# Kernel optimization log

Hardware: AMD Instinct MI355X
Metric: run time of the kernel (lower is better)

## Reference

```python
import jax, jax.numpy as jnp
import numpy as np
from jax import lax

B, D, H, FF, M = 256, 256, 8, 1024, 2048
HD = D // H
SCALE = 1.0 / np.sqrt(HD).astype(np.float32)
THR, MOM, LR = 0.5, 0.9, 0.1


def setup_inputs() -> dict:
    key = jax.random.key(0)
    ks = jax.random.split(key, 8)
    w = lambda k, sh: jax.random.normal(k, sh, dtype=jnp.float32) * 0.02
    return {
        "src": jax.random.normal(ks[0], (B, D), dtype=jnp.float32),
        "memory": jax.random.normal(ks[1], (M, D), dtype=jnp.float32) * 0.1,
        "momentum": jnp.zeros((M, D), jnp.float32),
        "scores": jax.random.uniform(ks[2], (M,), dtype=jnp.float32),
        "in_proj_w": w(ks[3], (3 * D, D)), "in_proj_b": jnp.zeros((3 * D,), jnp.float32),
        "out_w": w(ks[4], (D, D)), "out_b": jnp.zeros((D,), jnp.float32),
        "w1": w(ks[5], (FF, D)), "b1": jnp.zeros((FF,), jnp.float32),
        "w2": w(ks[6], (D, FF)), "b2": jnp.zeros((D,), jnp.float32),
        "g1": jnp.ones((D,), jnp.float32), "be1": jnp.zeros((D,), jnp.float32),
        "g2": jnp.ones((D,), jnp.float32), "be2": jnp.zeros((D,), jnp.float32),
        "ptr": M,
    }


def _ln(x, g, b):
    m = x.mean(-1, keepdims=True)
    v = ((x - m) ** 2).mean(-1, keepdims=True)
    return (x - m) / jnp.sqrt(v + 1e-5) * g + b


def reference(src, memory, momentum, scores, in_proj_w, in_proj_b, out_w, out_b,
              w1, b1, w2, b2, g1, be1, g2, be2, ptr):
    # --- surprise: 1 - max cosine similarity to memory slots ---
    xn = src / jnp.maximum(jnp.linalg.norm(src, axis=-1, keepdims=True), 1e-8)
    mn = memory / jnp.maximum(jnp.linalg.norm(memory, axis=-1, keepdims=True), 1e-8)
    sims = xn @ mn.T                                    # [B, M]
    surprises = jnp.where(jnp.linalg.norm(memory) == 0.0,
                          jnp.ones((B,), src.dtype), 1.0 - sims.max(-1))
    # --- self-attention; only the last (src) query row is used ---
    Wq, Wk, Wv = jnp.split(in_proj_w, 3, axis=0)
    bq, bk, bv = jnp.split(in_proj_b, 3, axis=0)
    q = (src @ Wq.T + bq).reshape(B, H, HD)             # [B,H,HD]
    k_mem = (memory @ Wk.T + bk).reshape(M, H, HD)      # shared across batch
    v_mem = (memory @ Wv.T + bv).reshape(M, H, HD)
    k_src = (src @ Wk.T + bk).reshape(B, H, HD)
    v_src = (src @ Wv.T + bv).reshape(B, H, HD)
    logits_mem = jnp.einsum('bhd,mhd->bhm', q, k_mem) * SCALE   # [B,H,M]
    logit_self = (q * k_src).sum(-1) * SCALE                    # [B,H]
    logits = jnp.concatenate([logits_mem, logit_self[..., None]], -1)  # [B,H,M+1]
    attn = jax.nn.softmax(logits, axis=-1)
    ctx = jnp.einsum('bhm,mhd->bhd', attn[..., :M], v_mem) + attn[..., M, None] * v_src
    attn_out = ctx.reshape(B, D) @ out_w.T + out_b
    h = _ln(src + attn_out, g1, be1)
    # --- sequential memory scatter update (detached in original) ---
    x_det = lax.stop_gradient(h)
    s_det = lax.stop_gradient(surprises)

    def step(carry, inp):
        mem, mom, sc, p = carry
        xi, si = inp
        cond = (si > THR) | (p < M)
        idx = jnp.mod(p, M)
        diff = xi - mem[idx]
        new_mom = MOM * mom[idx] + (1.0 - MOM) * diff
        mem = mem.at[idx].add(jnp.where(cond, LR * new_mom, 0.0))
        mom = mom.at[idx].set(jnp.where(cond, new_mom, mom[idx]))
        sc = sc.at[idx].set(jnp.where(cond, si, sc[idx]))
        return (mem, mom, sc, p + cond.astype(jnp.int32)), None

    (mem_f, mom_f, sc_f, _), _ = lax.scan(
        step, (memory, momentum, scores, jnp.int32(ptr)), (x_det, s_det))
    # --- FFN ---
    ff = jax.nn.relu(h @ w1.T + b1) @ w2.T + b2
    out = _ln(h + ff, g2, be2)
    return out, mem_f, mom_f, sc_f
```

## Files before the change

kernel.cpp:

```cpp
#include <hip/hip_runtime.h>
#include <math.h>

#define SCALE_F 0.17677669529663687f

typedef __attribute__((ext_vector_type(8))) short short8;
typedef __attribute__((ext_vector_type(4))) short short4v;
typedef __attribute__((ext_vector_type(4))) float f32x4;

__device__ inline short tobf(float x) {
    unsigned u = __float_as_uint(x);
    unsigned r = (u + 0x7FFFu + ((u >> 16) & 1u)) >> 16;
    return (short)r;
}
__device__ inline float frombf(short s) {
    return __uint_as_float(((unsigned)(unsigned short)s) << 16);
}

__device__ __forceinline__ short8 cv8(const float* __restrict__ p, int lo) {
    float4 a = *(const float4*)p, b = *(const float4*)(p + 4);
    float xs[8] = {a.x, a.y, a.z, a.w, b.x, b.y, b.z, b.w};
    short8 o;
    #pragma unroll
    for (int i = 0; i < 8; i++) {
        short hi = tobf(xs[i]);
        o[i] = lo ? tobf(xs[i] - frombf(hi)) : hi;
    }
    return o;
}

__device__ __forceinline__ void gemm_cv(short* lds,
    const float* __restrict__ A, int lda, int aLo,
    const float* __restrict__ B, int ldb, int bLo,
    float* Cf, short* Cb, int ldc, const float* bias, int transC, int bx, int by)
{
    short* Al = lds;
    short* Bl = lds + 2560;
    int t = threadIdx.x, w = t >> 6, l = t & 63;
    int r0 = by * 64, c0 = bx * 64;
    int srow = t >> 2, scol = (t & 3) * 8;
    f32x4 acc[4] = {{0.f,0.f,0.f,0.f},{0.f,0.f,0.f,0.f},{0.f,0.f,0.f,0.f},{0.f,0.f,0.f,0.f}};
    for (int kk = 0; kk < 256; kk += 32) {
        *(short8*)&Al[srow * 40 + scol] = cv8(A + (long long)(r0 + srow) * lda + kk + scol, aLo);
        *(short8*)&Bl[srow * 40 + scol] = cv8(B + (long long)(c0 + srow) * ldb + kk + scol, bLo);
        __syncthreads();
        short8 af = *(const short8*)&Al[(w * 16 + (l & 15)) * 40 + (l >> 4) * 8];
        #pragma unroll
        for (int j = 0; j < 4; j++) {
            short8 bf = *(const short8*)&Bl[(j * 16 + (l & 15)) * 40 + (l >> 4) * 8];
            acc[j] = __builtin_amdgcn_mfma_f32_16x16x32_bf16(af, bf, acc[j], 0, 0, 0);
        }
        __syncthreads();
    }
    int lc = l & 15, lr = (l >> 4) * 4;
    #pragma unroll
    for (int j = 0; j < 4; j++) {
        int col = c0 + j * 16 + lc;
        float bv = bias ? bias[col] : 0.f;
        #pragma unroll
        for (int r = 0; r < 4; r++) {
            int row = r0 + w * 16 + lr + r;
            float v = acc[j][r] + bv;
            long long idx = transC ? (long long)col * ldc + row : (long long)row * ldc + col;
            if (Cf) Cf[idx] = v;
            else    Cb[idx] = tobf(v);
        }
    }
}

__global__ __launch_bounds__(256) void proj_k(
    const float* __restrict__ src, const float* __restrict__ memory,
    const float* __restrict__ ipw, const float* __restrict__ ipb,
    const float* __restrict__ out_w, const float* __restrict__ w1, const float* __restrict__ w2,
    float* __restrict__ simdot_p, short* __restrict__ qkv_bf,
    short* __restrict__ k_bf, short* __restrict__ vt_bf,
    short* __restrict__ outw_bf, short* __restrict__ w1_bf, short* __restrict__ w2_bf,
    float* __restrict__ nx, float* __restrict__ nm, float* __restrict__ nm2)
{
    __shared__ short lds[5120];
    int bid = blockIdx.x, t = threadIdx.x, w = t >> 6, l = t & 63;
    if (bid < 384) {
        int tm = bid >> 7, r = bid & 127;
        int aLo = (tm == 2), bLo = (tm == 1);
        gemm_cv(lds, src, 256, aLo, memory, 256, bLo,
                simdot_p + (long long)tm * 524288, nullptr, 2048, nullptr, 0, r & 31, r >> 5);
    } else if (bid < 512) {
        int r = bid - 384;
        gemm_cv(lds, memory, 256, 0, ipw + 65536, 256, 0,
                nullptr, k_bf, 256, ipb + 256, 0, r & 3, r >> 2);
    } else if (bid < 640) {
        int r = bid - 512;
        gemm_cv(lds, memory, 256, 0, ipw + 131072, 256, 0,
                nullptr, vt_bf, 2048, ipb + 512, 1, r & 3, r >> 2);
    } else if (bid < 688) {
        int r = bid - 640;
        gemm_cv(lds, src, 256, 0, ipw, 256, 0,
                nullptr, qkv_bf, 768, ipb, 0, r % 12, r / 12);
    } else if (bid < 724) {
        int nb = bid - 688;
        #pragma unroll
        for (int i = 0; i < 16; i++) {
            int r = nb * 64 + i * 4 + w;
            bool issrc = r < 256;
            int rr = issrc ? r : r - 256;
            const float* rowp = issrc ? src + (long long)rr * 256 : memory + (long long)rr * 256;
            float4 x = *(const float4*)(rowp + l * 4);
            float ss = x.x * x.x + x.y * x.y + x.z * x.z + x.w * x.w;
            #pragma unroll
            for (int m = 32; m; m >>= 1) ss += __shfl_xor(ss, m, 64);
            if (l == 0) {
                if (issrc) nx[rr] = fmaxf(sqrtf(ss), 1e-8f);
                else { nm[rr] = fmaxf(sqrtf(ss), 1e-8f); nm2[rr] = ss; }
            }
        }
    } else {
        long long base = (long long)(bid - 724) * 4096 + t * 8;
        #pragma unroll
        for (int rep = 0; rep < 2; rep++) {
            long long e = base + rep * 2048;
            const float* sp; short* dp; long long off;
            if (e < 65536)       { sp = out_w; dp = outw_bf; off = e; }
            else if (e < 327680) { sp = w1;    dp = w1_bf;   off = e - 65536; }
            else                 { sp = w2;    dp = w2_bf;   off = e - 327680; }
            *(short8*)&dp[off] = cv8(sp + off, 0);
        }
    }
}

__global__ __launch_bounds__(256) void flash_sur_k(
    const short* __restrict__ qkv_bf, const short* __restrict__ k_bf,
    const short* __restrict__ vt_bf,
    float* __restrict__ pvpart, float* __restrict__ mpart, float* __restrict__ lpart,
    const float* __restrict__ simdot_p, const float* __restrict__ nx,
    const float* __restrict__ nm, const float* __restrict__ nm2, float* __restrict__ sur)
{
    __shared__ __align__(16) short smem[22016];
    int bid = blockIdx.x, t = threadIdx.x;
    if (bid >= 256) {
        float* red = (float*)smem;
        int b = bid - 256;
        float tot = 0.f;
        for (int m = t; m < 2048; m += 256) tot += nm2[m];
        red[t] = tot; __syncthreads();
        for (int s = 128; s; s >>= 1) { if (t < s) red[t] += red[t + s]; __syncthreads(); }
        float total = red[0];
        __syncthreads();
        float invx = 1.f / nx[b];
        float mx = -1e30f;
        for (int m = t; m < 2048; m += 256) {
            long long i = (long long)b * 2048 + m;
            float d = simdot_p[i] + simdot_p[524288 + i] + simdot_p[1048576 + i];
            mx = fmaxf(mx, d * invx / nm[m]);
        }
        red[t] = mx; __syncthreads();
        for (int s = 128; s; s >>= 1) { if (t < s) red[t] = fmaxf(red[t], red[t + s]); __syncthreads(); }
        if (t == 0) sur[b] = (total == 0.f) ? 1.f : 1.f - red[0];
        return;
    }
    int ms = bid & 7, h = (bid >> 3) & 7, qt = bid >> 6;
    int q0 = qt * 64, m0 = ms * 256;
    int S = bid & 63;
    int w = t >> 6, l = t & 63;
    short* Kl = smem;
    short* Pl = smem + 5120;
    short8 af = *(const short8*)(qkv_bf + (q0 + w * 16 + (l & 15)) * 768 + h * 32 + (l >> 4) * 8);
    f32x4 accL[16];
    #pragma unroll
    for (int j = 0; j < 16; j++) accL[j] = f32x4{0.f, 0.f, 0.f, 0.f};
    #pragma unroll
    for (int half = 0; half < 2; half++) {
        #pragma unroll
        for (int s = 0; s < 2; s++) {
            int seg = t + s * 256; int row = seg >> 2, off = (seg & 3) * 8;
            *(short8*)&Kl[row * 40 + off] =
                *(const short8*)(k_bf + (long long)(m0 + half * 128 + row) * 256 + h * 32 + off);
        }
        __syncthreads();
        #pragma unroll
        for (int j = 0; j < 8; j++) {
            short8 bf = *(const short8*)&Kl[(j * 16 + (l & 15)) * 40 + (l >> 4) * 8];
            accL[half * 8 + j] = __builtin_amdgcn_mfma_f32_16x16x32_bf16(af, bf, accL[half * 8 + j], 0, 0, 0);
        }
        __syncthreads();
    }
    int r4 = (l >> 4) * 4;
    float mloc[4], lsum[4];
    #pragma unroll
    for (int r = 0; r < 4; r++) {
        float mx = -1e30f;
        #pragma unroll
        for (int j = 0; j < 16; j++) mx = fmaxf(mx, accL[j][r] * SCALE_F);
        #pragma unroll
        for (int msk = 1; msk < 16; msk <<= 1) mx = fmaxf(mx, __shfl_xor(mx, msk, 64));
        mloc[r] = mx;
    }
    #pragma unroll
    for (int j = 0; j < 16; j++)
        #pragma unroll
        for (int r = 0; r < 4; r++)
            accL[j][r] = __expf(accL[j][r] * SCALE_F - mloc[r]);
    #pragma unroll
    for (int r = 0; r < 4; r++) {
        float ls = 0.f;
        #pragma unroll
        for (int j = 0; j < 16; j++) ls += accL[j][r];
        #pragma unroll
        for (int msk = 1; msk < 16; msk <<= 1) ls += __shfl_xor(ls, msk, 64);
        lsum[r] = ls;
    }
    if ((l & 15) == 0) {
        #pragma unroll
        for (int r = 0; r < 4; r++) {
            int gq = q0 + w * 16 + r4 + r;
            mpart[S * 256 + gq] = mloc[r];
            lpart[S * 256 + gq] = lsum[r];
        }
    }
    #pragma unroll
    for (int j = 0; j < 16; j++)
        #pragma unroll
        for (int r = 0; r < 4; r++)
            Pl[(w * 16 + r4 + r) * 264 + j * 16 + (l & 15)] = tobf(accL[j][r]);
    __syncthreads();
    f32x4 accP[2] = {{0.f,0.f,0.f,0.f},{0.f,0.f,0.f,0.f}};
    #pragma unroll
    for (int ks = 0; ks < 8; ks++) {
        short8 pa = *(const short8*)&Pl[(w * 16 + (l & 15)) * 264 + ks * 32 + (l >> 4) * 8];
        #pragma unroll
        for (int df = 0; df < 2; df++) {
            short8 vb = *(const short8*)(vt_bf + (long long)(h * 32 + df * 16 + (l & 15)) * 2048
                                         + m0 + ks * 32 + (l >> 4) * 8);
            accP[df] = __builtin_amdgcn_mfma_f32_16x16x32_bf16(pa, vb, accP[df], 0, 0, 0);
        }
    }
    #pragma unroll
    for (int df = 0; df < 2; df++)
        #pragma unroll
        for (int r = 0; r < 4; r++) {
            int gq = q0 + w * 16 + r4 + r;
            pvpart[((long long)S * 256 + gq) * 32 + df * 16 + (l & 15)] = accP[df][r];
        }
}

__global__ __launch_bounds__(256) void attn_gemm_k(
    const short* __restrict__ qkv_bf, const float* __restrict__ mpart,
    const float* __restrict__ lpart, const float* __restrict__ pvpart,
    const short* __restrict__ outw_bf, float* __restrict__ attn_part,
    const float* __restrict__ sur, const int* __restrict__ ptr, int* __restrict__ inv)
{
    __shared__ float ws_n[64][8];
    __shared__ float es_n[64];
    __shared__ short Al[2560];
    __shared__ short Bl[2560];
    int j = blockIdx.x, t = threadIdx.x;
    if (j >= 128) {
        int* ired = (int*)ws_n;
        for (int m = t; m < 2048; m += 256) inv[m] = -1;
        float s = sur[t];
        int p0 = ptr[0];
        int thresh = 2048 - p0;
        bool cond = (t < thresh) || (s > 0.5f);
        unsigned long long ball = __ballot(cond);
        int lane = t & 63, wv = t >> 6;
        if (lane == 0) ired[wv] = __popcll(ball);
        __syncthreads();
        int off = 0;
        for (int i = 0; i < wv; i++) off += ired[i];
        int rank = off + __popcll(ball & ((1ULL << lane) - 1ULL));
        if (cond) inv[(p0 + rank) & 2047] = t;
        return;
    }
    int h = j >> 4, r = j & 15, bx = r & 3, by = r >> 2;
    int b0 = by * 64, c0 = bx * 64;
    #pragma unroll
    for (int p = 0; p < 8; p++) {
        int rl = p * 8 + (t >> 5);
        int lane32 = t & 31;
        int b = b0 + rl;
        float q = frombf(qkv_bf[b * 768 + h * 32 + lane32]);
        float k = frombf(qkv_bf[b * 768 + 256 + h * 32 + lane32]);
        float prod = q * k;
        #pragma unroll
        for (int m = 16; m; m >>= 1) prod += __shfl_xor(prod, m, 64);
        float sl = prod * SCALE_F;
        if (lane32 < 8) {
            int S = h * 8 + lane32;
            float msv = mpart[S * 256 + b];
            float lpv = lpart[S * 256 + b];
            float mx = msv;
            #pragma unroll
            for (int m = 4; m; m >>= 1) mx = fmaxf(mx, __shfl_xor(mx, m, 64));
            float Mf = fmaxf(mx, sl);
            float wgt = __expf(msv - Mf);
            float suml = wgt * lpv;
            #pragma unroll
            for (int m = 4; m; m >>= 1) suml += __shfl_xor(suml, m, 64);
            float Es = __expf(sl - Mf);
            float Ls = suml + Es;
            ws_n[rl][lane32] = wgt / Ls;
            if (lane32 == 0) es_n[rl] = Es / Ls;
        }
    }
    __syncthreads();
    {
        int rl = t >> 2, cg = (t & 3) * 8;
        int b = b0 + rl;
        short8 vs8 = *(const short8*)(qkv_bf + b * 768 + 512 + h * 32 + cg);
        float es = es_n[rl];
        float a8[8];
        #pragma unroll
        for (int d = 0; d < 8; d++) a8[d] = es * frombf(vs8[d]);
        #pragma unroll
        for (int s = 0; s < 8; s++) {
            float wn = ws_n[rl][s];
            const float* pvb = pvpart + ((long long)(h * 8 + s) * 256 + b) * 32 + cg;
            float4 p0 = *(const float4*)pvb;
            float4 p1 = *(const float4*)(pvb + 4);
            a8[0] += wn * p0.x; a8[1] += wn * p0.y; a8[2] += wn * p0.z; a8[3] += wn * p0.w;
            a8[4] += wn * p1.x; a8[5] += wn * p1.y; a8[6] += wn * p1.z; a8[7] += wn * p1.w;
        }
        short8 o = {tobf(a8[0]), tobf(a8[1]), tobf(a8[2]), tobf(a8[3]),
                    tobf(a8[4]), tobf(a8[5]), tobf(a8[6]), tobf(a8[7])};
        *(short8*)&Al[rl * 40 + cg] = o;
        *(short8*)&Bl[rl * 40 + cg] = *(const short8*)(outw_bf + (long long)(c0 + rl) * 256 + h * 32 + cg);
    }
    __syncthreads();
    int w = t >> 6, l = t & 63;
    short8 af = *(const short8*)&Al[(w * 16 + (l & 15)) * 40 + (l >> 4) * 8];
    f32x4 acc[4] = {{0.f,0.f,0.f,0.f},{0.f,0.f,0.f,0.f},{0.f,0.f,0.f,0.f},{0.f,0.f,0.f,0.f}};
    #pragma unroll
    for (int j4 = 0; j4 < 4; j4++) {
        short8 bf = *(const short8*)&Bl[(j4 * 16 + (l & 15)) * 40 + (l >> 4) * 8];
        acc[j4] = __builtin_amdgcn_mfma_f32_16x16x32_bf16(af, bf, acc[j4], 0, 0, 0);
    }
    int lc = l & 15, lr = (l >> 4) * 4;
    #pragma unroll
    for (int j4 = 0; j4 < 4; j4++) {
        int col = c0 + j4 * 16 + lc;
        #pragma unroll
        for (int rr = 0; rr < 4; rr++) {
            int row = b0 + w * 16 + lr + rr;
            attn_part[(long long)h * 65536 + row * 256 + col] = acc[j4][rr];
        }
    }
}

__global__ __launch_bounds__(256) void ff1_ln_k(
    const float* __restrict__ attn_part, const float* __restrict__ out_b,
    const float* __restrict__ src, const float* __restrict__ g1,
    const float* __restrict__ be1, const short* __restrict__ w1_bf,
    const float* __restrict__ b1, float* __restrict__ hbuf, short* __restrict__ ff1_bf)
{
    __shared__ short Afull[64 * 264];
    __shared__ short Bl[2560];
    int bx = blockIdx.x, by = blockIdx.y;
    int t = threadIdx.x, w = t >> 6, l = t & 63;
    #pragma unroll
    for (int p = 0; p < 16; p++) {
        int rl = p * 4 + w;
        int r = by * 64 + rl;
        int c = l * 4;
        float4 x = *(const float4*)(out_b + c);
        float4 sv = *(const float4*)(src + (long long)r * 256 + c);
        x.x += sv.x; x.y += sv.y; x.z += sv.z; x.w += sv.w;
        #pragma unroll
        for (int pp = 0; pp < 8; pp++) {
            float4 a = *(const float4*)(attn_part + (long long)pp * 65536 + r * 256 + c);
            x.x += a.x; x.y += a.y; x.z += a.z; x.w += a.w;
        }
        float s = x.x + x.y + x.z + x.w;
        #pragma unroll
        for (int m = 32; m; m >>= 1) s += __shfl_xor(s, m, 64);
        float mean = s * (1.f / 256.f);
        float4 cv = {x.x - mean, x.y - mean, x.z - mean, x.w - mean};
        float ss = cv.x * cv.x + cv.y * cv.y + cv.z * cv.z + cv.w * cv.w;
        #pragma unroll
        for (int m = 32; m; m >>= 1) ss += __shfl_xor(ss, m, 64);
        float rstd = rsqrtf(ss * (1.f / 256.f) + 1e-5f);
        float4 gg = *(const float4*)(g1 + c);
        float4 bb = *(const float4*)(be1 + c);
        float4 y = {cv.x * rstd * gg.x + bb.x, cv.y * rstd * gg.y + bb.y,
                    cv.z * rstd * gg.z + bb.z, cv.w * rstd * gg.w + bb.w};
        if (bx == 0) *(float4*)(hbuf + (long long)r * 256 + c) = y;
        short4v yb = {tobf(y.x), tobf(y.y), tobf(y.z), tobf(y.w)};
        *(short4v*)&Afull[rl * 264 + c] = yb;
    }
    __syncthreads();
    int c0 = bx * 64;
    int srow = t >> 2, scol = (t & 3) * 8;
    f32x4 acc[4] = {{0.f,0.f,0.f,0.f},{0.f,0.f,0.f,0.f},{0.f,0.f,0.f,0.f},{0.f,0.f,0.f,0.f}};
    for (int kk = 0; kk < 256; kk += 32) {
        *(short8*)&Bl[srow * 40 + scol] = *(const short8*)(w1_bf + (long long)(c0 + srow) * 256 + kk + scol);
        __syncthreads();
        short8 af = *(const short8*)&Afull[(w * 16 + (l & 15)) * 264 + kk + (l >> 4) * 8];
        #pragma unroll
        for (int j = 0; j < 4; j++) {
            short8 bf = *(const short8*)&Bl[(j * 16 + (l & 15)) * 40 + (l >> 4) * 8];
            acc[j] = __builtin_amdgcn_mfma_f32_16x16x32_bf16(af, bf, acc[j], 0, 0, 0);
        }
        __syncthreads();
    }
    int lc = l & 15, lr = (l >> 4) * 4;
    #pragma unroll
    for (int j = 0; j < 4; j++) {
        int col = c0 + j * 16 + lc;
        float bv = b1[col];
        #pragma unroll
        for (int r = 0; r < 4; r++) {
            int row = by * 64 + w * 16 + lr + r;
            float v = fmaxf(acc[j][r] + bv, 0.f);
            ff1_bf[(long long)row * 1024 + col] = tobf(v);
        }
    }
}

__device__ __forceinline__ void gemm_tile(short* lds,
    const short* __restrict__ A, int lda, const short* __restrict__ B, int ldb,
    float* Cf, int ldc, long long coff, int Klen, int kbeg, int bx, int by)
{
    short* Al = lds;
    short* Bl = lds + 2560;
    int t = threadIdx.x, w = t >> 6, l = t & 63;
    int r0 = by * 64, c0 = bx * 64;
    int srow = t >> 2, scol = (t & 3) * 8;
    f32x4 acc[4] = {{0.f,0.f,0.f,0.f},{0.f,0.f,0.f,0.f},{0.f,0.f,0.f,0.f},{0.f,0.f,0.f,0.f}};
    for (int kk = 0; kk < Klen; kk += 32) {
        int k0 = kbeg + kk;
        *(short8*)&Al[srow * 40 + scol] = *(const short8*)(A + (long long)(r0 + srow) * lda + k0 + scol);
        *(short8*)&Bl[srow * 40 + scol] = *(const short8*)(B + (long long)(c0 + srow) * ldb + k0 + scol);
        __syncthreads();
        short8 af = *(const short8*)&Al[(w * 16 + (l & 15)) * 40 + (l >> 4) * 8];
        #pragma unroll
        for (int j = 0; j < 4; j++) {
            short8 bf = *(const short8*)&Bl[(j * 16 + (l & 15)) * 40 + (l >> 4) * 8];
            acc[j] = __builtin_amdgcn_mfma_f32_16x16x32_bf16(af, bf, acc[j], 0, 0, 0);
        }
        __syncthreads();
    }
    int lc = l & 15, lr = (l >> 4) * 4;
    #pragma unroll
    for (int j = 0; j < 4; j++) {
        int col = c0 + j * 16 + lc;
        #pragma unroll
        for (int r = 0; r < 4; r++) {
            int row = r0 + w * 16 + lr + r;
            Cf[coff + (long long)row * ldc + col] = acc[j][r];
        }
    }
}

__global__ __launch_bounds__(256) void ff2_mem_k(
    const short* __restrict__ ff1_bf, const short* __restrict__ w2_bf,
    float* __restrict__ ff2_part,
    const float* __restrict__ memory, const float* __restrict__ momentum,
    const float* __restrict__ scores, const float* __restrict__ hbuf,
    const float* __restrict__ sur, const int* __restrict__ inv,
    float* __restrict__ mem_o, float* __restrict__ mom_o, float* __restrict__ sc_o)
{
    __shared__ short lds[5120];
    int j = blockIdx.x, t = threadIdx.x;
    if (j < 128) {
        int ks = j >> 4, r = j & 15;
        gemm_tile(lds, ff1_bf, 1024, w2_bf, 1024, ff2_part, 256,
                  (long long)ks * 65536, 128, ks * 128, r & 3, r >> 2);
        return;
    }
    int w = t >> 6, l = t & 63;
    int m = (j - 128) * 4 + w;
    int b = inv[m];
    long long o = (long long)m * 256 + l * 4;
    float4 xm = *(const float4*)(memory + o);
    float4 mo = *(const float4*)(momentum + o);
    if (b >= 0) {
        float4 hb = *(const float4*)(hbuf + (long long)b * 256 + l * 4);
        float4 nmom = {0.9f * mo.x + 0.1f * (hb.x - xm.x), 0.9f * mo.y + 0.1f * (hb.y - xm.y),
                       0.9f * mo.z + 0.1f * (hb.z - xm.z), 0.9f * mo.w + 0.1f * (hb.w - xm.w)};
        float4 nm4 = {xm.x + 0.1f * nmom.x, xm.y + 0.1f * nmom.y,
                      xm.z + 0.1f * nmom.z, xm.w + 0.1f * nmom.w};
        *(float4*)(mem_o + o) = nm4;
        *(float4*)(mom_o + o) = nmom;
        if (l == 0) sc_o[m] = sur[b];
    } else {
        *(float4*)(mem_o + o) = xm;
        *(float4*)(mom_o + o) = mo;
        if (l == 0) sc_o[m] = scores[m];
    }
}

__global__ __launch_bounds__(256) void ln2_k(
    const float* __restrict__ ff2_part, const float* __restrict__ b2,
    const float* __restrict__ hbuf, const float* __restrict__ g2,
    const float* __restrict__ be2, float* __restrict__ out_main)
{
    int t = threadIdx.x, w = t >> 6, l = t & 63;
    int r = blockIdx.x * 4 + w;
    int c = l * 4;
    float4 x = *(const float4*)(b2 + c);
    float4 hv = *(const float4*)(hbuf + (long long)r * 256 + c);
    x.x += hv.x; x.y += hv.y; x.z += hv.z; x.w += hv.w;
    #pragma unroll
    for (int pp = 0; pp < 8; pp++) {
        float4 a = *(const float4*)(ff2_part + (long long)pp * 65536 + r * 256 + c);
        x.x += a.x; x.y += a.y; x.z += a.z; x.w += a.w;
    }
    float s = x.x + x.y + x.z + x.w;
    #pragma unroll
    for (int m = 32; m; m >>= 1) s += __shfl_xor(s, m, 64);
    float mean = s * (1.f / 256.f);
    float4 cv = {x.x - mean, x.y - mean, x.z - mean, x.w - mean};
    float ss = cv.x * cv.x + cv.y * cv.y + cv.z * cv.z + cv.w * cv.w;
    #pragma unroll
    for (int m = 32; m; m >>= 1) ss += __shfl_xor(ss, m, 64);
    float rstd = rsqrtf(ss * (1.f / 256.f) + 1e-5f);
    float4 gg = *(const float4*)(g2 + c);
    float4 bb = *(const float4*)(be2 + c);
    float4 y = {cv.x * rstd * gg.x + bb.x, cv.y * rstd * gg.y + bb.y,
                cv.z * rstd * gg.z + bb.z, cv.w * rstd * gg.w + bb.w};
    *(float4*)(out_main + (long long)r * 256 + c) = y;
}

extern "C" void kernel_launch(void* const* d_in, const int* in_sizes, int n_in,
                              void* d_out, int out_size, void* d_ws, size_t ws_size,
                              hipStream_t stream)
{
    const float* src      = (const float*)d_in[0];
    const float* memory   = (const float*)d_in[1];
    const float* momentum = (const float*)d_in[2];
    const float* scores   = (const float*)d_in[3];
    const float* ipw      = (const float*)d_in[4];
    const float* ipb      = (const float*)d_in[5];
    const float* out_w    = (const float*)d_in[6];
    const float* out_b    = (const float*)d_in[7];
    const float* w1       = (const float*)d_in[8];
    const float* b1       = (const float*)d_in[9];
    const float* w2       = (const float*)d_in[10];
    const float* b2       = (const float*)d_in[11];
    const float* g1       = (const float*)d_in[12];
    const float* be1      = (const float*)d_in[13];
    const float* g2       = (const float*)d_in[14];
    const float* be2      = (const float*)d_in[15];
    const int*   ptr      = (const int*)d_in[16];

    float* o = (float*)d_out;
    float* out_main = o;
    float* mem_o = o + 65536;
    float* mom_o = mem_o + 524288;
    float* sc_o  = mom_o + 524288;

    char* wp = (char*)d_ws;
    auto alloc = [&](size_t n) { void* q = (void*)wp; wp += (n + 255) & ~(size_t)255; return q; };
    short* qkv_bf   = (short*)alloc(393216);
    short* k_bf     = (short*)alloc(1048576);
    short* vt_bf    = (short*)alloc(1048576);
    short* outw_bf  = (short*)alloc(131072);
    short* w1_bf    = (short*)alloc(524288);
    short* w2_bf    = (short*)alloc(524288);
    short* ff1_bf   = (short*)alloc(524288);
    float* simdot_p = (float*)alloc(6291456);
    float* pvpart   = (float*)alloc(2097152);
    float* mpart    = (float*)alloc(65536);
    float* lpart    = (float*)alloc(65536);
    float* attn_part= (float*)alloc(2097152);
    float* ff2_part = (float*)alloc(2097152);
    float* hbuf     = (float*)alloc(262144);
    float* nx       = (float*)alloc(1024);
    float* nm       = (float*)alloc(8192);
    float* nm2      = (float*)alloc(8192);
    float* sur      = (float*)alloc(1024);
    int*   inv      = (int*)alloc(8192);

    proj_k<<<868, 256, 0, stream>>>(src, memory, ipw, ipb, out_w, w1, w2,
        simdot_p, qkv_bf, k_bf, vt_bf, outw_bf, w1_bf, w2_bf, nx, nm, nm2);
    flash_sur_k<<<512, 256, 0, stream>>>(qkv_bf, k_bf, vt_bf, pvpart, mpart, lpart,
        simdot_p, nx, nm, nm2, sur);
    attn_gemm_k<<<129, 256, 0, stream>>>(qkv_bf, mpart, lpart, pvpart, outw_bf,
        attn_part, sur, ptr, inv);
    ff1_ln_k<<<dim3(16, 4), 256, 0, stream>>>(attn_part, out_b, src, g1, be1,
        w1_bf, b1, hbuf, ff1_bf);
    ff2_mem_k<<<640, 256, 0, stream>>>(ff1_bf, w2_bf, ff2_part,
        memory, momentum, scores, hbuf, sur, inv, mem_o, mom_o, sc_o);
    ln2_k<<<64, 256, 0, stream>>>(ff2_part, b2, hbuf, g2, be2, out_main);
}
```

Before: 145.9 us.

## Drop split-bf16 similarity GEMM and halve FF1 row tiles for more blocks

The cosine-similarity GEMM previously used a three-pass hi/lo bf16 split to approximate fp32 precision. It now runs a single bf16 pass and writes one similarity buffer instead of three partials. This cuts 256 GEMM blocks and the reads of the partials in the surprise reduction. The FF1+LN kernel now uses 32-row tiles over a 16x8 grid, with warps split 2x2, to raise block count. The risk is that the lower precision of the max-cosine can flip surprise threshold decisions near 0.5, which changes which memory slots get updated.

```diff
diff --git a/kernel.cpp b/kernel.cpp
--- a/kernel.cpp
+++ b/kernel.cpp
@@ -16,21 +16,16 @@
     return __uint_as_float(((unsigned)(unsigned short)s) << 16);
 }
 
-__device__ __forceinline__ short8 cv8(const float* __restrict__ p, int lo) {
+__device__ __forceinline__ short8 cv8(const float* __restrict__ p) {
     float4 a = *(const float4*)p, b = *(const float4*)(p + 4);
-    float xs[8] = {a.x, a.y, a.z, a.w, b.x, b.y, b.z, b.w};
-    short8 o;
-    #pragma unroll
-    for (int i = 0; i < 8; i++) {
-        short hi = tobf(xs[i]);
-        o[i] = lo ? tobf(xs[i] - frombf(hi)) : hi;
-    }
+    short8 o = {tobf(a.x), tobf(a.y), tobf(a.z), tobf(a.w),
+                tobf(b.x), tobf(b.y), tobf(b.z), tobf(b.w)};
     return o;
 }
 
 __device__ __forceinline__ void gemm_cv(short* lds,
-    const float* __restrict__ A, int lda, int aLo,
-    const float* __restrict__ B, int ldb, int bLo,
+    const float* __restrict__ A, int lda,
+    const float* __restrict__ B, int ldb,
     float* Cf, short* Cb, int ldc, const float* bias, int transC, int bx, int by)
 {
     short* Al = lds;
@@ -40,8 +35,8 @@
     int srow = t >> 2, scol = (t & 3) * 8;
     f32x4 acc[4] = {{0.f,0.f,0.f,0.f},{0.f,0.f,0.f,0.f},{0.f,0.f,0.f,0.f},{0.f,0.f,0.f,0.f}};
     for (int kk = 0; kk < 256; kk += 32) {
-        *(short8*)&Al[srow * 40 + scol] = cv8(A + (long long)(r0 + srow) * lda + kk + scol, aLo);
-        *(short8*)&Bl[srow * 40 + scol] = cv8(B + (long long)(c0 + srow) * ldb + kk + scol, bLo);
+        *(short8*)&Al[srow * 40 + scol] = cv8(A + (long long)(r0 + srow) * lda + kk + scol);
+        *(short8*)&Bl[srow * 40 + scol] = cv8(B + (long long)(c0 + srow) * ldb + kk + scol);
         __syncthreads();
         short8 af = *(const short8*)&Al[(w * 16 + (l & 15)) * 40 + (l >> 4) * 8];
         #pragma unroll
@@ -71,32 +66,30 @@
     const float* __restrict__ src, const float* __restrict__ memory,
     const float* __restrict__ ipw, const float* __restrict__ ipb,
     const float* __restrict__ out_w, const float* __restrict__ w1, const float* __restrict__ w2,
-    float* __restrict__ simdot_p, short* __restrict__ qkv_bf,
+    float* __restrict__ simdot, short* __restrict__ qkv_bf,
     short* __restrict__ k_bf, short* __restrict__ vt_bf,
     short* __restrict__ outw_bf, short* __restrict__ w1_bf, short* __restrict__ w2_bf,
     float* __restrict__ nx, float* __restrict__ nm, float* __restrict__ nm2)
 {
     __shared__ short lds[5120];
     int bid = blockIdx.x, t = threadIdx.x, w = t >> 6, l = t & 63;
-    if (bid < 384) {
-        int tm = bid >> 7, r = bid & 127;
-        int aLo = (tm == 2), bLo = (tm == 1);
-        gemm_cv(lds, src, 256, aLo, memory, 256, bLo,
-                simdot_p + (long long)tm * 524288, nullptr, 2048, nullptr, 0, r & 31, r >> 5);
-    } else if (bid < 512) {
+    if (bid < 128) {
+        gemm_cv(lds, src, 256, memory, 256,
+                simdot, nullptr, 2048, nullptr, 0, bid & 31, bid >> 5);
+    } else if (bid < 256) {
+        int r = bid - 128;
+        gemm_cv(lds, memory, 256, ipw + 65536, 256,
+                nullptr, k_bf, 256, ipb + 256, 0, r & 3, r >> 2);
+    } else if (bid < 384) {
+        int r = bid - 256;
+        gemm_cv(lds, memory, 256, ipw + 131072, 256,
+                nullptr, vt_bf, 2048, ipb + 512, 1, r & 3, r >> 2);
+    } else if (bid < 432) {
         int r = bid - 384;
-        gemm_cv(lds, memory, 256, 0, ipw + 65536, 256, 0,
-                nullptr, k_bf, 256, ipb + 256, 0, r & 3, r >> 2);
-    } else if (bid < 640) {
-        int r = bid - 512;
-        gemm_cv(lds, memory, 256, 0, ipw + 131072, 256, 0,
-                nullptr, vt_bf, 2048, ipb + 512, 1, r & 3, r >> 2);
-    } else if (bid < 688) {
-        int r = bid - 640;
-        gemm_cv(lds, src, 256, 0, ipw, 256, 0,
+        gemm_cv(lds, src, 256, ipw, 256,
                 nullptr, qkv_bf, 768, ipb, 0, r % 12, r / 12);
-    } else if (bid < 724) {
-        int nb = bid - 688;
+    } else if (bid < 468) {
+        int nb = bid - 432;
         #pragma unroll
         for (int i = 0; i < 16; i++) {
             int r = nb * 64 + i * 4 + w;
@@ -113,7 +106,7 @@
             }
         }
     } else {
-        long long base = (long long)(bid - 724) * 4096 + t * 8;
+        long long base = (long long)(bid - 468) * 4096 + t * 8;
         #pragma unroll
         for (int rep = 0; rep < 2; rep++) {
             long long e = base + rep * 2048;
@@ -121,7 +114,7 @@
             if (e < 65536)       { sp = out_w; dp = outw_bf; off = e; }
             else if (e < 327680) { sp = w1;    dp = w1_bf;   off = e - 65536; }
             else                 { sp = w2;    dp = w2_bf;   off = e - 327680; }
-            *(short8*)&dp[off] = cv8(sp + off, 0);
+            *(short8*)&dp[off] = cv8(sp + off);
         }
     }
 }
@@ -130,7 +123,7 @@
     const short* __restrict__ qkv_bf, const short* __restrict__ k_bf,
     const short* __restrict__ vt_bf,
     float* __restrict__ pvpart, float* __restrict__ mpart, float* __restrict__ lpart,
-    const float* __restrict__ simdot_p, const float* __restrict__ nx,
+    const float* __restrict__ simdot, const float* __restrict__ nx,
     const float* __restrict__ nm, const float* __restrict__ nm2, float* __restrict__ sur)
 {
     __shared__ __align__(16) short smem[22016];
@@ -147,8 +140,7 @@
         float invx = 1.f / nx[b];
         float mx = -1e30f;
         for (int m = t; m < 2048; m += 256) {
-            long long i = (long long)b * 2048 + m;
-            float d = simdot_p[i] + simdot_p[524288 + i] + simdot_p[1048576 + i];
+            float d = simdot[(long long)b * 2048 + m];
             mx = fmaxf(mx, d * invx / nm[m]);
         }
         red[t] = mx; __syncthreads();
@@ -350,14 +342,14 @@
     const float* __restrict__ be1, const short* __restrict__ w1_bf,
     const float* __restrict__ b1, float* __restrict__ hbuf, short* __restrict__ ff1_bf)
 {
-    __shared__ short Afull[64 * 264];
+    __shared__ short Afull[32 * 264];
     __shared__ short Bl[2560];
     int bx = blockIdx.x, by = blockIdx.y;
     int t = threadIdx.x, w = t >> 6, l = t & 63;
     #pragma unroll
-    for (int p = 0; p < 16; p++) {
+    for (int p = 0; p < 8; p++) {
         int rl = p * 4 + w;
-        int r = by * 64 + rl;
+        int r = by * 32 + rl;
         int c = l * 4;
         float4 x = *(const float4*)(out_b + c);
         float4 sv = *(const float4*)(src + (long long)r * 256 + c);
@@ -387,27 +379,29 @@
     __syncthreads();
     int c0 = bx * 64;
     int srow = t >> 2, scol = (t & 3) * 8;
-    f32x4 acc[4] = {{0.f,0.f,0.f,0.f},{0.f,0.f,0.f,0.f},{0.f,0.f,0.f,0.f},{0.f,0.f,0.f,0.f}};
+    int wr = w & 1, wc = w >> 1;
+    f32x4 acc[2] = {{0.f,0.f,0.f,0.f},{0.f,0.f,0.f,0.f}};
     for (int kk = 0; kk < 256; kk += 32) {
         *(short8*)&Bl[srow * 40 + scol] = *(const short8*)(w1_bf + (long long)(c0 + srow) * 256 + kk + scol);
         __syncthreads();
-        short8 af = *(const short8*)&Afull[(w * 16 + (l & 15)) * 264 + kk + (l >> 4) * 8];
-        #pragma unroll
-        for (int j = 0; j < 4; j++) {
+        short8 af = *(const short8*)&Afull[(wr * 16 + (l & 15)) * 264 + kk + (l >> 4) * 8];
+        #pragma unroll
+        for (int jj = 0; jj < 2; jj++) {
+            int j = wc * 2 + jj;
             short8 bf = *(const short8*)&Bl[(j * 16 + (l & 15)) * 40 + (l >> 4) * 8];
-            acc[j] = __builtin_amdgcn_mfma_f32_16x16x32_bf16(af, bf, acc[j], 0, 0, 0);
+            acc[jj] = __builtin_amdgcn_mfma_f32_16x16x32_bf16(af, bf, acc[jj], 0, 0, 0);
         }
         __syncthreads();
     }
     int lc = l & 15, lr = (l >> 4) * 4;
     #pragma unroll
-    for (int j = 0; j < 4; j++) {
-        int col = c0 + j * 16 + lc;
+    for (int jj = 0; jj < 2; jj++) {
+        int col = c0 + (wc * 2 + jj) * 16 + lc;
         float bv = b1[col];
         #pragma unroll
         for (int r = 0; r < 4; r++) {
-            int row = by * 64 + w * 16 + lr + r;
-            float v = fmaxf(acc[j][r] + bv, 0.f);
+            int row = by * 32 + wr * 16 + lr + r;
+            float v = fmaxf(acc[jj][r] + bv, 0.f);
             ff1_bf[(long long)row * 1024 + col] = tobf(v);
         }
     }
@@ -555,7 +549,7 @@
     short* w1_bf    = (short*)alloc(524288);
     short* w2_bf    = (short*)alloc(524288);
     short* ff1_bf   = (short*)alloc(524288);
-    float* simdot_p = (float*)alloc(6291456);
+    float* simdot   = (float*)alloc(2097152);
     float* pvpart   = (float*)alloc(2097152);
     float* mpart    = (float*)alloc(65536);
     float* lpart    = (float*)alloc(65536);
@@ -568,13 +562,13 @@
     float* sur      = (float*)alloc(1024);
     int*   inv      = (int*)alloc(8192);
 
-    proj_k<<<868, 256, 0, stream>>>(src, memory, ipw, ipb, out_w, w1, w2,
-        simdot_p, qkv_bf, k_bf, vt_bf, outw_bf, w1_bf, w2_bf, nx, nm, nm2);
+    proj_k<<<612, 256, 0, stream>>>(src, memory, ipw, ipb, out_w, w1, w2,
+        simdot, qkv_bf, k_bf, vt_bf, outw_bf, w1_bf, w2_bf, nx, nm, nm2);
     flash_sur_k<<<512, 256, 0, stream>>>(qkv_bf, k_bf, vt_bf, pvpart, mpart, lpart,
-        simdot_p, nx, nm, nm2, sur);
+        simdot, nx, nm, nm2, sur);
     attn_gemm_k<<<129, 256, 0, stream>>>(qkv_bf, mpart, lpart, pvpart, outw_bf,
         attn_part, sur, ptr, inv);
-    ff1_ln_k<<<dim3(16, 4), 256, 0, stream>>>(attn_part, out_b, src, g1, be1,
+    ff1_ln_k<<<dim3(16, 8), 256, 0, stream>>>(attn_part, out_b, src, g1, be1,
         w1_bf, b1, hbuf, ff1_bf);
     ff2_mem_k<<<640, 256, 0, stream>>>(ff1_bf, w2_bf, ff2_part,
         memory, momentum, scores, hbuf, sur, inv, mem_o, mom_o, sc_o);
```

Result: faster. 137.7 us (-5.7%).
